# Optimization experiments

Measured on AMD Instinct MI355X. Metric: run time of the kernel, lower is better.

Reference implementation:

```python
import jax, jax.numpy as jnp
import numpy as np

B_, N_, DM = 4, 4096, 256
DS, DC = 16, 4
DIN = DM * 1          # expand = 1
DTR = (DM + 15) // 16  # dt_rank = ceil(d_model/16) = 16


def setup_inputs() -> dict:
    key = jax.random.key(0)
    ks = jax.random.split(key, 8)
    s = lambda k, shape, sc=0.02: jax.random.normal(k, shape, jnp.float32) * sc
    return {
        "x": jax.random.normal(ks[0], (B_, N_, DM), jnp.float32),
        "W_in": s(ks[1], (DM, 2 * DIN)),                 # in_proj (no bias)
        "conv_w": s(ks[2], (DIN, DC), 0.1),              # depthwise causal conv
        "conv_b": jnp.zeros((DIN,), jnp.float32),
        "W_xproj": s(ks[3], (DIN, DTR + 2 * DS)),        # x_proj (no bias)
        "W_dt": s(ks[4], (DTR, DIN), 0.1),               # dt_proj weight
        "b_dt": jnp.full((DIN,), -4.0, jnp.float32),     # dt_proj bias (softplus -> small dt)
        "A_log": jnp.log(jnp.broadcast_to(jnp.arange(1, DS + 1, dtype=jnp.float32), (DIN, DS))),
        "D": jnp.ones((DIN,), jnp.float32),              # skip connection
        "W_out": s(ks[5], (DIN, DM)),                    # out_proj (no bias)
        "H": 64,
        "W": 64,
    }


def _mamba(x, W_in, conv_w, conv_b, W_xproj, W_dt, b_dt, A_log, D, W_out):
    # x: [B, L, d_model]
    B, L, _ = x.shape
    xz = x @ W_in                                   # [B, L, 2*DIN]
    xc, z = jnp.split(xz, 2, axis=-1)
    # causal depthwise conv1d over L
    xt = jnp.transpose(xc, (0, 2, 1))               # [B, DIN, L]
    rhs = conv_w[:, None, :]                        # [DIN, 1, K]
    conv = jax.lax.conv_general_dilated(
        xt, rhs, (1,), [(DC - 1, 0)],
        dimension_numbers=("NCH", "OIH", "NCH"), feature_group_count=DIN)
    xc = jax.nn.silu(jnp.transpose(conv, (0, 2, 1)) + conv_b)   # [B, L, DIN]
    # input-dependent SSM parameters
    dbl = xc @ W_xproj                              # [B, L, DTR+2*DS]
    dt, Bm, Cm = jnp.split(dbl, [DTR, DTR + DS], axis=-1)
    delta = jax.nn.softplus(dt @ W_dt + b_dt)       # [B, L, DIN]
    A = -jnp.exp(A_log)                             # [DIN, DS]
    dA = jnp.exp(delta[..., None] * A)              # [B, L, DIN, DS]
    dBx = delta[..., None] * Bm[:, :, None, :] * xc[..., None]  # [B, L, DIN, DS]

    def step(h, inputs):
        dA_t, dBx_t, C_t = inputs                   # [B,DIN,DS],[B,DIN,DS],[B,DS]
        h = dA_t * h + dBx_t
        y = jnp.einsum("bds,bs->bd", h, C_t)
        return h, y

    h0 = jnp.zeros((B, DIN, DS), x.dtype)
    _, ys = jax.lax.scan(step, h0,
                         (jnp.moveaxis(dA, 1, 0), jnp.moveaxis(dBx, 1, 0), jnp.moveaxis(Cm, 1, 0)))
    y = jnp.moveaxis(ys, 0, 1)                      # [B, L, DIN]
    y = (y + D * xc) * jax.nn.silu(z)
    return y @ W_out                                # [B, L, d_model]


def reference(x, W_in, conv_w, conv_b, W_xproj, W_dt, b_dt, A_log, D, W_out, H, W):
    B, N, C = x.shape
    m = lambda t: _mamba(t, W_in, conv_w, conv_b, W_xproj, W_dt, b_dt, A_log, D, W_out)
    out_h_fwd = m(x)
    out_h_bwd = jnp.flip(m(jnp.flip(x, axis=1)), axis=1)
    x_v = x.reshape(B, H, W, C).transpose(0, 2, 1, 3).reshape(B, N, C)
    out_v_fwd = m(x_v).reshape(B, W, H, C).transpose(0, 2, 1, 3).reshape(B, N, C)
    out_v_bwd = jnp.flip(m(jnp.flip(x_v, axis=1)), axis=1)
    out_v_bwd = out_v_bwd.reshape(B, W, H, C).transpose(0, 2, 1, 3).reshape(B, N, C)
    out = (out_h_fwd + out_h_bwd + out_v_fwd + out_v_bwd) / 4.0
    out = jnp.clip(out, -1000.0, 1000.0)
    return jnp.nan_to_num(out, nan=0.0, posinf=1000.0, neginf=-1000.0)
```

## Files before the change

### kernel.cpp

```cpp
#include <hip/hip_runtime.h>
#include <cmath>

constexpr int BB = 4;
constexpr int LL = 4096;
constexpr int CH = 32;
constexpr int NC = LL / CH;
constexpr size_t EL = (size_t)BB * LL * 256;

typedef __attribute__((ext_vector_type(8))) short bf16x8;
typedef __attribute__((ext_vector_type(4))) float f32x4;

__device__ __forceinline__ int dirmap(int dir, int p) {
    switch (dir) {
        case 0: return p;
        case 1: return (LL - 1) - p;
        case 2: return ((p & 63) << 6) | (p >> 6);
        default: { int q = (LL - 1) - p; return ((q & 63) << 6) | (q >> 6); }
    }
}

__device__ __forceinline__ float silu_f(float v) {
    return v * __builtin_amdgcn_rcpf(1.f + __expf(-v));
}
__device__ __forceinline__ float softplus_f(float v) {
    const float sp = __logf(1.f + __expf(v));
    return (v > 20.f) ? v : sp;
}
__device__ __forceinline__ unsigned short f2bf(float f) {
    unsigned int u = __float_as_uint(f);
    return (unsigned short)((u + 0x7FFFu + ((u >> 16) & 1u)) >> 16);
}
__device__ __forceinline__ float bf2f(unsigned short s) {
    return __uint_as_float(((unsigned int)s) << 16);
}

__global__ __launch_bounds__(256) void split_x_k(
    const float* __restrict__ src, unsigned short* __restrict__ h,
    unsigned short* __restrict__ l, int n4)
{
    const int i = blockIdx.x * 256 + threadIdx.x;
    if (i >= n4) return;
    const float4 v = reinterpret_cast<const float4*>(src)[i];
    ushort4 hv, lv;
    hv.x = f2bf(v.x); lv.x = f2bf(v.x - bf2f(hv.x));
    hv.y = f2bf(v.y); lv.y = f2bf(v.y - bf2f(hv.y));
    hv.z = f2bf(v.z); lv.z = f2bf(v.z - bf2f(hv.z));
    hv.w = f2bf(v.w); lv.w = f2bf(v.w - bf2f(hv.w));
    reinterpret_cast<ushort4*>(h)[i] = hv;
    reinterpret_cast<ushort4*>(l)[i] = lv;
}

__global__ __launch_bounds__(256) void tsplit_k(
    const float* __restrict__ W, unsigned short* __restrict__ Th,
    unsigned short* __restrict__ Tl, int N)
{
    const int n = blockIdx.x;
    const int k = threadIdx.x;
    const float v = W[(size_t)k * N + n];
    const unsigned short h = f2bf(v);
    Th[(size_t)n * 256 + k] = h;
    Tl[(size_t)n * 256 + k] = f2bf(v - bf2f(h));
}

__global__ __launch_bounds__(256) void split_acc_k(
    const float* __restrict__ acc4, const float* __restrict__ zs,
    unsigned short* __restrict__ h, unsigned short* __restrict__ l, int n4)
{
    const int i = blockIdx.x * 256 + threadIdx.x;
    if (i >= n4) return;
    const float4 a0 = reinterpret_cast<const float4*>(acc4)[i];
    const float4 a1 = reinterpret_cast<const float4*>(acc4 + EL)[i];
    const float4 a2 = reinterpret_cast<const float4*>(acc4 + 2 * EL)[i];
    const float4 a3 = reinterpret_cast<const float4*>(acc4 + 3 * EL)[i];
    const float4 z = reinterpret_cast<const float4*>(zs)[i];
    float4 v;
    v.x = (a0.x + a1.x + a2.x + a3.x) * z.x * 0.25f;
    v.y = (a0.y + a1.y + a2.y + a3.y) * z.y * 0.25f;
    v.z = (a0.z + a1.z + a2.z + a3.z) * z.z * 0.25f;
    v.w = (a0.w + a1.w + a2.w + a3.w) * z.w * 0.25f;
    ushort4 hv, lv;
    hv.x = f2bf(v.x); lv.x = f2bf(v.x - bf2f(hv.x));
    hv.y = f2bf(v.y); lv.y = f2bf(v.y - bf2f(hv.y));
    hv.z = f2bf(v.z); lv.z = f2bf(v.z - bf2f(hv.z));
    hv.w = f2bf(v.w); lv.w = f2bf(v.w - bf2f(hv.w));
    reinterpret_cast<ushort4*>(h)[i] = hv;
    reinterpret_cast<ushort4*>(l)[i] = lv;
}

template<int EPI>
__global__ __launch_bounds__(256, 4) void gemm_mfma(
    const unsigned short* __restrict__ Ah, const unsigned short* __restrict__ Al,
    const unsigned short* __restrict__ BTh, const unsigned short* __restrict__ BTl,
    float* __restrict__ out0, float* __restrict__ out1)
{
    constexpr int LDT = 40;
    __shared__ unsigned short AhS[128 * LDT], AlS[128 * LDT];
    __shared__ unsigned short BhS[64 * LDT], BlS[64 * LDT];

    const int tid = threadIdx.x;
    const int wave = tid >> 6, lane = tid & 63;
    const int lm = lane & 15, quad = lane >> 4;
    const int m0 = blockIdx.y * 128, n0 = blockIdx.x * 64;

    const int srow = tid >> 2;
    const int scol = (tid & 3) * 8;

    f32x4 acc[2][4];
#pragma unroll
    for (int mt = 0; mt < 2; mt++)
#pragma unroll
        for (int nt = 0; nt < 4; nt++)
#pragma unroll
            for (int e = 0; e < 4; e++) acc[mt][nt][e] = 0.f;

    for (int k0 = 0; k0 < 256; k0 += 32) {
#pragma unroll
        for (int hh = 0; hh < 2; hh++) {
            const int r = srow + hh * 64;
            const size_t g = (size_t)(m0 + r) * 256 + k0 + scol;
            *reinterpret_cast<int4*>(&AhS[r * LDT + scol]) =
                *reinterpret_cast<const int4*>(&Ah[g]);
            *reinterpret_cast<int4*>(&AlS[r * LDT + scol]) =
                *reinterpret_cast<const int4*>(&Al[g]);
        }
        {
            const size_t g = (size_t)(n0 + srow) * 256 + k0 + scol;
            *reinterpret_cast<int4*>(&BhS[srow * LDT + scol]) =
                *reinterpret_cast<const int4*>(&BTh[g]);
            *reinterpret_cast<int4*>(&BlS[srow * LDT + scol]) =
                *reinterpret_cast<const int4*>(&BTl[g]);
        }
        __syncthreads();

        const int ko = quad * 8;
        bf16x8 a_h[2], a_l[2], b_h[4], b_l[4];
#pragma unroll
        for (int mt = 0; mt < 2; mt++) {
            const int r = wave * 32 + mt * 16 + lm;
            a_h[mt] = *reinterpret_cast<const bf16x8*>(&AhS[r * LDT + ko]);
            a_l[mt] = *reinterpret_cast<const bf16x8*>(&AlS[r * LDT + ko]);
        }
#pragma unroll
        for (int nt = 0; nt < 4; nt++) {
            const int r = nt * 16 + lm;
            b_h[nt] = *reinterpret_cast<const bf16x8*>(&BhS[r * LDT + ko]);
            b_l[nt] = *reinterpret_cast<const bf16x8*>(&BlS[r * LDT + ko]);
        }
#pragma unroll
        for (int mt = 0; mt < 2; mt++)
#pragma unroll
            for (int nt = 0; nt < 4; nt++) {
                acc[mt][nt] = __builtin_amdgcn_mfma_f32_16x16x32_bf16(
                    a_h[mt], b_h[nt], acc[mt][nt], 0, 0, 0);
                acc[mt][nt] = __builtin_amdgcn_mfma_f32_16x16x32_bf16(
                    a_h[mt], b_l[nt], acc[mt][nt], 0, 0, 0);
                acc[mt][nt] = __builtin_amdgcn_mfma_f32_16x16x32_bf16(
                    a_l[mt], b_h[nt], acc[mt][nt], 0, 0, 0);
            }
        __syncthreads();
    }

#pragma unroll
    for (int mt = 0; mt < 2; mt++) {
#pragma unroll
        for (int nt = 0; nt < 4; nt++) {
            const int col = n0 + nt * 16 + lm;
#pragma unroll
            for (int r = 0; r < 4; r++) {
                const int row = m0 + wave * 32 + mt * 16 + quad * 4 + r;
                float v = acc[mt][nt][r];
                if (EPI == 0) {
                    if (n0 < 256) out0[(size_t)row * 256 + col] = v;
                    else          out1[(size_t)row * 256 + (col - 256)] = silu_f(v);
                } else {
                    v = fminf(fmaxf(v, -1000.f), 1000.f);
                    if (v != v) v = 0.f;
                    out0[(size_t)row * 256 + col] = v;
                }
            }
        }
    }
}

__global__ __launch_bounds__(256) void conv_all(
    const float* __restrict__ xc0, const float* __restrict__ conv_w,
    const float* __restrict__ conv_b, float* __restrict__ xcd)
{
    const int bx = blockIdx.x;
    const int g = bx >> 7;
    const int nc = bx & 127;
    const int dir = g >> 2, b = g & 3;
    const int p0 = nc * CH;
    const int d = threadIdx.x;
    const size_t xbase = ((size_t)b << 12) * 256;

    const float4 cw = *reinterpret_cast<const float4*>(&conv_w[d * 4]);
    const float cb = conv_b[d];
    float xin[35];
#pragma unroll
    for (int i = 0; i < 35; i++) {
        const int p = p0 - 3 + i;
        xin[i] = (p >= 0) ? xc0[xbase + (size_t)dirmap(dir, p) * 256 + d] : 0.f;
    }
#pragma unroll
    for (int t = 0; t < 32; t++) {
        const float v = cb + cw.x * xin[t] + cw.y * xin[t + 1]
                           + cw.z * xin[t + 2] + cw.w * xin[t + 3];
        xcd[(((size_t)g << 12) + p0 + t) * 256 + d] = silu_f(v);
    }
}

__global__ __launch_bounds__(256, 2) void gemm_dbl(
    const float* __restrict__ xcd, const float* __restrict__ Wx,
    float* __restrict__ dtbc)
{
    __shared__ float Bs[256 * 48];
    __shared__ float As[16][132];

    const int tid = threadIdx.x;
    const int m0 = blockIdx.x * 128;
    const int ty = tid >> 3;
    const int tx = tid & 7;
    const int sr = tid >> 2;
    const int sc = (tid & 3) * 4;

#pragma unroll
    for (int i = 0; i < 12; i++)
        reinterpret_cast<float4*>(Bs)[tid + i * 256] =
            reinterpret_cast<const float4*>(Wx)[tid + i * 256];

    float acc[4][6];
#pragma unroll
    for (int i = 0; i < 4; i++)
#pragma unroll
        for (int j = 0; j < 6; j++) acc[i][j] = 0.f;

    for (int k0 = 0; k0 < 256; k0 += 16) {
#pragma unroll
        for (int h = 0; h < 2; h++) {
            const int r = sr + h * 64;
            const float4 av = *reinterpret_cast<const float4*>(
                &xcd[(size_t)(m0 + r) * 256 + k0 + sc]);
            As[sc + 0][r] = av.x; As[sc + 1][r] = av.y;
            As[sc + 2][r] = av.z; As[sc + 3][r] = av.w;
        }
        __syncthreads();
#pragma unroll
        for (int kk = 0; kk < 16; kk++) {
            const float4 a4 = *reinterpret_cast<const float4*>(&As[kk][ty * 4]);
            const float* brow = &Bs[(k0 + kk) * 48 + tx * 6];
            const float2 b0 = *reinterpret_cast<const float2*>(brow + 0);
            const float2 b1 = *reinterpret_cast<const float2*>(brow + 2);
            const float2 b2 = *reinterpret_cast<const float2*>(brow + 4);
            const float a[4] = {a4.x, a4.y, a4.z, a4.w};
            const float bb[6] = {b0.x, b0.y, b1.x, b1.y, b2.x, b2.y};
#pragma unroll
            for (int i = 0; i < 4; i++)
#pragma unroll
                for (int j = 0; j < 6; j++)
                    acc[i][j] = fmaf(a[i], bb[j], acc[i][j]);
        }
        __syncthreads();
    }
#pragma unroll
    for (int i = 0; i < 4; i++) {
        float* orow = &dtbc[(size_t)(m0 + ty * 4 + i) * 48 + tx * 6];
#pragma unroll
        for (int j = 0; j < 3; j++)
            *reinterpret_cast<float2*>(orow + j * 2) =
                make_float2(acc[i][j * 2], acc[i][j * 2 + 1]);
    }
}

__global__ __launch_bounds__(256) void passA2(
    const float* __restrict__ xcd, const float* __restrict__ dtbc,
    const float* __restrict__ Wdt, const float* __restrict__ bdt,
    float* __restrict__ qbuf, float* __restrict__ ssum)
{
    __shared__ float dts[32 * 48];
    const int bx = blockIdx.x;
    const int g = bx >> 7;
    const int nc = bx & 127;
    const int p0 = nc * CH;
    const int d = threadIdx.x;

    {
        const float4* src = reinterpret_cast<const float4*>(
            &dtbc[(((size_t)g << 12) + p0) * 48]);
        float4* dst = reinterpret_cast<float4*>(dts);
        dst[d] = src[d];
        if (d < 128) dst[256 + d] = src[256 + d];
    }

    float wdt[16];
#pragma unroll
    for (int r = 0; r < 16; r++) wdt[r] = Wdt[r * 256 + d];
    const float bdt_d = bdt[d];
    __syncthreads();

    float hq[16];
#pragma unroll
    for (int s = 0; s < 16; s++) hq[s] = 0.f;
    float ss = 0.f;

    const float* xrow = &xcd[(((size_t)g << 12) + p0) * 256 + d];
    float xv = xrow[0];
    for (int t = 0; t < 32; t++) {
        const float xnext = xrow[(t + 1) * 256];
        const float* drow = &dts[t * 48];
        float dv = bdt_d;
#pragma unroll
        for (int r4 = 0; r4 < 4; r4++) {
            const float4 d4 = *reinterpret_cast<const float4*>(drow + r4 * 4);
            dv = fmaf(d4.x, wdt[r4 * 4 + 0], dv);
            dv = fmaf(d4.y, wdt[r4 * 4 + 1], dv);
            dv = fmaf(d4.z, wdt[r4 * 4 + 2], dv);
            dv = fmaf(d4.w, wdt[r4 * 4 + 3], dv);
        }
        const float de = softplus_f(dv);
        ss += de;
        const float e0 = __expf(-de);
        const float dx = de * xv;
        float pw = 1.f;
#pragma unroll
        for (int s4 = 0; s4 < 4; s4++) {
            const float4 b4 = *reinterpret_cast<const float4*>(drow + 16 + s4 * 4);
            pw *= e0; hq[s4 * 4 + 0] = fmaf(pw, hq[s4 * 4 + 0], dx * b4.x);
            pw *= e0; hq[s4 * 4 + 1] = fmaf(pw, hq[s4 * 4 + 1], dx * b4.y);
            pw *= e0; hq[s4 * 4 + 2] = fmaf(pw, hq[s4 * 4 + 2], dx * b4.z);
            pw *= e0; hq[s4 * 4 + 3] = fmaf(pw, hq[s4 * 4 + 3], dx * b4.w);
        }
        xv = xnext;
    }
    const size_t base = (size_t)bx * 256 + d;
    ssum[base] = ss;
    float4* qp = reinterpret_cast<float4*>(qbuf + base * 16);
#pragma unroll
    for (int s4 = 0; s4 < 4; s4++)
        qp[s4] = make_float4(hq[s4 * 4 + 0], hq[s4 * 4 + 1],
                             hq[s4 * 4 + 2], hq[s4 * 4 + 3]);
}

__global__ __launch_bounds__(256) void scanB_k(
    float* __restrict__ qs, const float* __restrict__ ssum)
{
    const int blk = blockIdx.x;
    const int gg = blk >> 4;
    const int dd = ((blk & 15) << 4) | (threadIdx.x >> 4);
    const int s = threadIdx.x & 15;
    const float msp1 = -(float)(s + 1);
    const size_t b0 = (size_t)gg * NC * 256 + dd;

    constexpr int PD = 8;
    float qv[PD], sv[PD];
#pragma unroll
    for (int j = 0; j < PD; j++) {
        qv[j] = qs[(b0 + (size_t)j * 256) * 16 + s];
        sv[j] = ssum[b0 + (size_t)j * 256];
    }
    float h = 0.f;
    for (int nc = 0; nc < NC; nc += PD) {
        const int pn = (nc + PD < NC) ? nc + PD : nc;
        float qn[PD], sn[PD];
#pragma unroll
        for (int j = 0; j < PD; j++) {
            qn[j] = qs[(b0 + (size_t)(pn + j) * 256) * 16 + s];
            sn[j] = ssum[b0 + (size_t)(pn + j) * 256];
        }
#pragma unroll
        for (int j = 0; j < PD; j++) {
            qs[(b0 + (size_t)(nc + j) * 256) * 16 + s] = h;
            h = fmaf(__expf(msp1 * sv[j]), h, qv[j]);
        }
#pragma unroll
        for (int j = 0; j < PD; j++) { qv[j] = qn[j]; sv[j] = sn[j]; }
    }
}

__global__ __launch_bounds__(256) void passC3(
    const float* __restrict__ xcd, const float* __restrict__ dtbc,
    const float* __restrict__ Wdt, const float* __restrict__ bdt,
    const float* __restrict__ Dv, const float* __restrict__ hinit,
    float* __restrict__ acc4)
{
    __shared__ float dts[32 * 48];
    const int bx = blockIdx.x;
    const int g = bx >> 7;
    const int nc = bx & 127;
    const int dir = g >> 2, b = g & 3;
    const int p0 = nc * CH;
    const int d = threadIdx.x;
    float* accd = acc4 + (size_t)dir * EL + ((size_t)b << 12) * 256;

    {
        const float4* src = reinterpret_cast<const float4*>(
            &dtbc[(((size_t)g << 12) + p0) * 48]);
        float4* dst = reinterpret_cast<float4*>(dts);
        dst[d] = src[d];
        if (d < 128) dst[256 + d] = src[256 + d];
    }

    float wdt[16];
#pragma unroll
    for (int r = 0; r < 16; r++) wdt[r] = Wdt[r * 256 + d];
    const float bdt_d = bdt[d];
    const float Dd = Dv[d];

    float hq[16];
    const float4* hp = reinterpret_cast<const float4*>(
        hinit + (((size_t)g * NC + nc) * 256 + d) * 16);
#pragma unroll
    for (int s4 = 0; s4 < 4; s4++) {
        const float4 hv = hp[s4];
        hq[s4 * 4 + 0] = hv.x; hq[s4 * 4 + 1] = hv.y;
        hq[s4 * 4 + 2] = hv.z; hq[s4 * 4 + 3] = hv.w;
    }
    __syncthreads();

    const int nbase = dirmap(dir, p0);
    const int nstep = (dir == 0) ? 1 : (dir == 1) ? -1 : (dir == 2) ? 64 : -64;
    float* op = accd + (size_t)nbase * 256 + d;
    const ptrdiff_t ostep = (ptrdiff_t)nstep * 256;

    const float* xrow = &xcd[(((size_t)g << 12) + p0) * 256 + d];
    float xv = xrow[0];
    for (int t = 0; t < 32; t++) {
        const float xnext = xrow[(t + 1) * 256];
        const float* drow = &dts[t * 48];
        float dv = bdt_d;
#pragma unroll
        for (int r4 = 0; r4 < 4; r4++) {
            const float4 d4 = *reinterpret_cast<const float4*>(drow + r4 * 4);
            dv = fmaf(d4.x, wdt[r4 * 4 + 0], dv);
            dv = fmaf(d4.y, wdt[r4 * 4 + 1], dv);
            dv = fmaf(d4.z, wdt[r4 * 4 + 2], dv);
            dv = fmaf(d4.w, wdt[r4 * 4 + 3], dv);
        }
        const float de = softplus_f(dv);
        const float e0 = __expf(-de);
        const float dx = de * xv;
        float y = 0.f, pw = 1.f;
#pragma unroll
        for (int s4 = 0; s4 < 4; s4++) {
            const float4 b4 = *reinterpret_cast<const float4*>(drow + 16 + s4 * 4);
            const float4 c4 = *reinterpret_cast<const float4*>(drow + 32 + s4 * 4);
            pw *= e0; hq[s4 * 4 + 0] = fmaf(pw, hq[s4 * 4 + 0], dx * b4.x);
            y = fmaf(hq[s4 * 4 + 0], c4.x, y);
            pw *= e0; hq[s4 * 4 + 1] = fmaf(pw, hq[s4 * 4 + 1], dx * b4.y);
            y = fmaf(hq[s4 * 4 + 1], c4.y, y);
            pw *= e0; hq[s4 * 4 + 2] = fmaf(pw, hq[s4 * 4 + 2], dx * b4.z);
            y = fmaf(hq[s4 * 4 + 2], c4.z, y);
            pw *= e0; hq[s4 * 4 + 3] = fmaf(pw, hq[s4 * 4 + 3], dx * b4.w);
            y = fmaf(hq[s4 * 4 + 3], c4.w, y);
        }
        *op = y + Dd * xv;
        op += ostep;
        xv = xnext;
    }
}

extern "C" void kernel_launch(void* const* d_in, const int* in_sizes, int n_in,
                              void* d_out, int out_size, void* d_ws, size_t ws_size,
                              hipStream_t stream) {
    const float* x      = (const float*)d_in[0];
    const float* W_in   = (const float*)d_in[1];
    const float* conv_w = (const float*)d_in[2];
    const float* conv_b = (const float*)d_in[3];
    const float* W_xprj = (const float*)d_in[4];
    const float* W_dt   = (const float*)d_in[5];
    const float* b_dt   = (const float*)d_in[6];
    const float* Dv     = (const float*)d_in[8];
    const float* W_out  = (const float*)d_in[9];
    float* out = (float*)d_out;

    char* ws = (char*)d_ws;
    size_t off = 0;
    auto alloc = [&](size_t bytes) {
        void* p = ws + off; off += (bytes + 255) & ~(size_t)255; return p;
    };
    float* acc4 = (float*)alloc(4 * EL * 4);
    unsigned short* xh  = (unsigned short*)acc4;
    unsigned short* xl  = xh + EL;
    float* xc0 = (float*)(xl + EL);
    float* zs   = (float*)alloc(EL * 4);
    float* xcd  = (float*)alloc(4 * EL * 4);
    float* dtbc = (float*)alloc((size_t)16 * LL * 48 * 4);
    float* qbuf = (float*)alloc((size_t)16 * NC * 256 * 16 * 4);
    float* ssumb = (float*)alloc((size_t)16 * NC * 256 * 4);
    unsigned short* WinTh = (unsigned short*)alloc(512 * 256 * 2);
    unsigned short* WinTl = (unsigned short*)alloc(512 * 256 * 2);
    unsigned short* WoutTh = (unsigned short*)alloc(256 * 256 * 2);
    unsigned short* WoutTl = (unsigned short*)alloc(256 * 256 * 2);
    unsigned short* ah = (unsigned short*)qbuf;
    unsigned short* al = ah + EL;

    split_x_k<<<4096, 256, 0, stream>>>(x, xh, xl, (int)(EL / 4));
    tsplit_k<<<512, 256, 0, stream>>>(W_in, WinTh, WinTl, 512);
    tsplit_k<<<256, 256, 0, stream>>>(W_out, WoutTh, WoutTl, 256);

    gemm_mfma<0><<<dim3(8, 128), 256, 0, stream>>>(
        xh, xl, WinTh, WinTl, xc0, zs);

    conv_all<<<2048, 256, 0, stream>>>(xc0, conv_w, conv_b, xcd);

    gemm_dbl<<<512, 256, 0, stream>>>(xcd, W_xprj, dtbc);

    passA2<<<2048, 256, 0, stream>>>(xcd, dtbc, W_dt, b_dt, qbuf, ssumb);

    scanB_k<<<256, 256, 0, stream>>>(qbuf, ssumb);

    passC3<<<2048, 256, 0, stream>>>(xcd, dtbc, W_dt, b_dt, Dv, qbuf, acc4);

    split_acc_k<<<4096, 256, 0, stream>>>(acc4, zs, ah, al, (int)(EL / 4));

    gemm_mfma<2><<<dim3(4, 128), 256, 0, stream>>>(
        ah, al, WoutTh, WoutTl, out, nullptr);
}
```

Before: 307.6 us.

## Fuse conv into consumers, fold x bf16 split into input GEMM, restructure scan math

Removes the separate split_x_k and conv_all kernels. The input GEMM now splits fp32 x into hi/lo bf16 while staging tiles into shared memory, and the causal conv plus SiLU is recomputed inside gemm_dbl, passA and passC instead of reading a materialized 4x-sized xcd buffer. The scan passes compute softplus via a single exp/rcp/log, precompute the 16 powers of exp(-delta) with a shallow product tree instead of a serial chain, and split the C-dot product into four accumulators for more ILP. This trades redundant conv recomputation and more register pressure for less global traffic and fewer launches.

New measurement: 378.3 us. 1.23x slower.

```diff
diff --git a/kernel.cpp b/kernel.cpp
--- a/kernel.cpp
+++ b/kernel.cpp
@@ -22,32 +22,12 @@
 __device__ __forceinline__ float silu_f(float v) {
     return v * __builtin_amdgcn_rcpf(1.f + __expf(-v));
 }
-__device__ __forceinline__ float softplus_f(float v) {
-    const float sp = __logf(1.f + __expf(v));
-    return (v > 20.f) ? v : sp;
-}
 __device__ __forceinline__ unsigned short f2bf(float f) {
     unsigned int u = __float_as_uint(f);
     return (unsigned short)((u + 0x7FFFu + ((u >> 16) & 1u)) >> 16);
 }
 __device__ __forceinline__ float bf2f(unsigned short s) {
     return __uint_as_float(((unsigned int)s) << 16);
-}
-
-__global__ __launch_bounds__(256) void split_x_k(
-    const float* __restrict__ src, unsigned short* __restrict__ h,
-    unsigned short* __restrict__ l, int n4)
-{
-    const int i = blockIdx.x * 256 + threadIdx.x;
-    if (i >= n4) return;
-    const float4 v = reinterpret_cast<const float4*>(src)[i];
-    ushort4 hv, lv;
-    hv.x = f2bf(v.x); lv.x = f2bf(v.x - bf2f(hv.x));
-    hv.y = f2bf(v.y); lv.y = f2bf(v.y - bf2f(hv.y));
-    hv.z = f2bf(v.z); lv.z = f2bf(v.z - bf2f(hv.z));
-    hv.w = f2bf(v.w); lv.w = f2bf(v.w - bf2f(hv.w));
-    reinterpret_cast<ushort4*>(h)[i] = hv;
-    reinterpret_cast<ushort4*>(l)[i] = lv;
 }
 
 __global__ __launch_bounds__(256) void tsplit_k(
@@ -87,9 +67,8 @@
     reinterpret_cast<ushort4*>(l)[i] = lv;
 }
 
-template<int EPI>
-__global__ __launch_bounds__(256, 4) void gemm_mfma(
-    const unsigned short* __restrict__ Ah, const unsigned short* __restrict__ Al,
+__global__ __launch_bounds__(256, 4) void gemm_in(
+    const float* __restrict__ A0,
     const unsigned short* __restrict__ BTh, const unsigned short* __restrict__ BTl,
     float* __restrict__ out0, float* __restrict__ out1)
 {
@@ -118,10 +97,22 @@
         for (int hh = 0; hh < 2; hh++) {
             const int r = srow + hh * 64;
             const size_t g = (size_t)(m0 + r) * 256 + k0 + scol;
-            *reinterpret_cast<int4*>(&AhS[r * LDT + scol]) =
-                *reinterpret_cast<const int4*>(&Ah[g]);
-            *reinterpret_cast<int4*>(&AlS[r * LDT + scol]) =
-                *reinterpret_cast<const int4*>(&Al[g]);
+            const float4 v0 = *reinterpret_cast<const float4*>(&A0[g]);
+            const float4 v1 = *reinterpret_cast<const float4*>(&A0[g + 4]);
+            const float v[8] = {v0.x, v0.y, v0.z, v0.w, v1.x, v1.y, v1.z, v1.w};
+            ushort4 ha, hb, la, lb;
+            ha.x = f2bf(v[0]); la.x = f2bf(v[0] - bf2f(ha.x));
+            ha.y = f2bf(v[1]); la.y = f2bf(v[1] - bf2f(ha.y));
+            ha.z = f2bf(v[2]); la.z = f2bf(v[2] - bf2f(ha.z));
+            ha.w = f2bf(v[3]); la.w = f2bf(v[3] - bf2f(ha.w));
+            hb.x = f2bf(v[4]); lb.x = f2bf(v[4] - bf2f(hb.x));
+            hb.y = f2bf(v[5]); lb.y = f2bf(v[5] - bf2f(hb.y));
+            hb.z = f2bf(v[6]); lb.z = f2bf(v[6] - bf2f(hb.z));
+            hb.w = f2bf(v[7]); lb.w = f2bf(v[7] - bf2f(hb.w));
+            *reinterpret_cast<ushort4*>(&AhS[r * LDT + scol]) = ha;
+            *reinterpret_cast<ushort4*>(&AhS[r * LDT + scol + 4]) = hb;
+            *reinterpret_cast<ushort4*>(&AlS[r * LDT + scol]) = la;
+            *reinterpret_cast<ushort4*>(&AlS[r * LDT + scol + 4]) = lb;
         }
         {
             const size_t g = (size_t)(n0 + srow) * 256 + k0 + scol;
@@ -168,61 +159,120 @@
 #pragma unroll
             for (int r = 0; r < 4; r++) {
                 const int row = m0 + wave * 32 + mt * 16 + quad * 4 + r;
+                const float v = acc[mt][nt][r];
+                if (n0 < 256) out0[(size_t)row * 256 + col] = v;
+                else          out1[(size_t)row * 256 + (col - 256)] = silu_f(v);
+            }
+        }
+    }
+}
+
+__global__ __launch_bounds__(256, 4) void gemm_out(
+    const unsigned short* __restrict__ Ah, const unsigned short* __restrict__ Al,
+    const unsigned short* __restrict__ BTh, const unsigned short* __restrict__ BTl,
+    float* __restrict__ out0)
+{
+    constexpr int LDT = 40;
+    __shared__ unsigned short AhS[128 * LDT], AlS[128 * LDT];
+    __shared__ unsigned short BhS[64 * LDT], BlS[64 * LDT];
+
+    const int tid = threadIdx.x;
+    const int wave = tid >> 6, lane = tid & 63;
+    const int lm = lane & 15, quad = lane >> 4;
+    const int m0 = blockIdx.y * 128, n0 = blockIdx.x * 64;
+
+    const int srow = tid >> 2;
+    const int scol = (tid & 3) * 8;
+
+    f32x4 acc[2][4];
+#pragma unroll
+    for (int mt = 0; mt < 2; mt++)
+#pragma unroll
+        for (int nt = 0; nt < 4; nt++)
+#pragma unroll
+            for (int e = 0; e < 4; e++) acc[mt][nt][e] = 0.f;
+
+    for (int k0 = 0; k0 < 256; k0 += 32) {
+#pragma unroll
+        for (int hh = 0; hh < 2; hh++) {
+            const int r = srow + hh * 64;
+            const size_t g = (size_t)(m0 + r) * 256 + k0 + scol;
+            *reinterpret_cast<int4*>(&AhS[r * LDT + scol]) =
+                *reinterpret_cast<const int4*>(&Ah[g]);
+            *reinterpret_cast<int4*>(&AlS[r * LDT + scol]) =
+                *reinterpret_cast<const int4*>(&Al[g]);
+        }
+        {
+            const size_t g = (size_t)(n0 + srow) * 256 + k0 + scol;
+            *reinterpret_cast<int4*>(&BhS[srow * LDT + scol]) =
+                *reinterpret_cast<const int4*>(&BTh[g]);
+            *reinterpret_cast<int4*>(&BlS[srow * LDT + scol]) =
+                *reinterpret_cast<const int4*>(&BTl[g]);
+        }
+        __syncthreads();
+
+        const int ko = quad * 8;
+        bf16x8 a_h[2], a_l[2], b_h[4], b_l[4];
+#pragma unroll
+        for (int mt = 0; mt < 2; mt++) {
+            const int r = wave * 32 + mt * 16 + lm;
+            a_h[mt] = *reinterpret_cast<const bf16x8*>(&AhS[r * LDT + ko]);
+            a_l[mt] = *reinterpret_cast<const bf16x8*>(&AlS[r * LDT + ko]);
+        }
+#pragma unroll
+        for (int nt = 0; nt < 4; nt++) {
+            const int r = nt * 16 + lm;
+            b_h[nt] = *reinterpret_cast<const bf16x8*>(&BhS[r * LDT + ko]);
+            b_l[nt] = *reinterpret_cast<const bf16x8*>(&BlS[r * LDT + ko]);
+        }
+#pragma unroll
+        for (int mt = 0; mt < 2; mt++)
+#pragma unroll
+            for (int nt = 0; nt < 4; nt++) {
+                acc[mt][nt] = __builtin_amdgcn_mfma_f32_16x16x32_bf16(
+                    a_h[mt], b_h[nt], acc[mt][nt], 0, 0, 0);
+                acc[mt][nt] = __builtin_amdgcn_mfma_f32_16x16x32_bf16(
+                    a_h[mt], b_l[nt], acc[mt][nt], 0, 0, 0);
+                acc[mt][nt] = __builtin_amdgcn_mfma_f32_16x16x32_bf16(
+                    a_l[mt], b_h[nt], acc[mt][nt], 0, 0, 0);
+            }
+        __syncthreads();
+    }
+
+#pragma unroll
+    for (int mt = 0; mt < 2; mt++) {
+#pragma unroll
+        for (int nt = 0; nt < 4; nt++) {
+            const int col = n0 + nt * 16 + lm;
+#pragma unroll
+            for (int r = 0; r < 4; r++) {
+                const int row = m0 + wave * 32 + mt * 16 + quad * 4 + r;
                 float v = acc[mt][nt][r];
-                if (EPI == 0) {
-                    if (n0 < 256) out0[(size_t)row * 256 + col] = v;
-                    else          out1[(size_t)row * 256 + (col - 256)] = silu_f(v);
-                } else {
-                    v = fminf(fmaxf(v, -1000.f), 1000.f);
-                    if (v != v) v = 0.f;
-                    out0[(size_t)row * 256 + col] = v;
-                }
+                v = fminf(fmaxf(v, -1000.f), 1000.f);
+                if (v != v) v = 0.f;
+                out0[(size_t)row * 256 + col] = v;
             }
         }
     }
 }
 
-__global__ __launch_bounds__(256) void conv_all(
+__global__ __launch_bounds__(256, 2) void gemm_dbl(
     const float* __restrict__ xc0, const float* __restrict__ conv_w,
-    const float* __restrict__ conv_b, float* __restrict__ xcd)
-{
-    const int bx = blockIdx.x;
-    const int g = bx >> 7;
-    const int nc = bx & 127;
-    const int dir = g >> 2, b = g & 3;
-    const int p0 = nc * CH;
-    const int d = threadIdx.x;
-    const size_t xbase = ((size_t)b << 12) * 256;
-
-    const float4 cw = *reinterpret_cast<const float4*>(&conv_w[d * 4]);
-    const float cb = conv_b[d];
-    float xin[35];
-#pragma unroll
-    for (int i = 0; i < 35; i++) {
-        const int p = p0 - 3 + i;
-        xin[i] = (p >= 0) ? xc0[xbase + (size_t)dirmap(dir, p) * 256 + d] : 0.f;
-    }
-#pragma unroll
-    for (int t = 0; t < 32; t++) {
-        const float v = cb + cw.x * xin[t] + cw.y * xin[t + 1]
-                           + cw.z * xin[t + 2] + cw.w * xin[t + 3];
-        xcd[(((size_t)g << 12) + p0 + t) * 256 + d] = silu_f(v);
-    }
-}
-
-__global__ __launch_bounds__(256, 2) void gemm_dbl(
-    const float* __restrict__ xcd, const float* __restrict__ Wx,
+    const float* __restrict__ conv_b, const float* __restrict__ Wx,
     float* __restrict__ dtbc)
 {
     __shared__ float Bs[256 * 48];
     __shared__ float As[16][132];
+    __shared__ float Xr[16][132];
 
     const int tid = threadIdx.x;
     const int m0 = blockIdx.x * 128;
+    const int g = m0 >> 12;
+    const int dir = g >> 2, b = g & 3;
+    const int p0 = m0 & 4095;
+    const size_t xbase = ((size_t)b << 12) * 256;
     const int ty = tid >> 3;
     const int tx = tid & 7;
-    const int sr = tid >> 2;
-    const int sc = (tid & 3) * 4;
 
 #pragma unroll
     for (int i = 0; i < 12; i++)
@@ -237,12 +287,29 @@
 
     for (int k0 = 0; k0 < 256; k0 += 16) {
 #pragma unroll
-        for (int h = 0; h < 2; h++) {
-            const int r = sr + h * 64;
-            const float4 av = *reinterpret_cast<const float4*>(
-                &xcd[(size_t)(m0 + r) * 256 + k0 + sc]);
-            As[sc + 0][r] = av.x; As[sc + 1][r] = av.y;
-            As[sc + 2][r] = av.z; As[sc + 3][r] = av.w;
+        for (int i = 0; i < 9; i++) {
+            const int idx = tid + i * 256;
+            if (idx < 131 * 16) {
+                const int k = idx & 15, pi = idx >> 4;
+                const int gp = p0 - 3 + pi;
+                float v = 0.f;
+                if (gp >= 0)
+                    v = xc0[xbase + (size_t)dirmap(dir, gp) * 256 + k0 + k];
+                Xr[k][pi] = v;
+            }
+        }
+        __syncthreads();
+#pragma unroll
+        for (int i = 0; i < 8; i++) {
+            const int idx = tid + i * 256;
+            const int k = idx & 15, r = idx >> 4;
+            const float4 cw = *reinterpret_cast<const float4*>(&conv_w[(k0 + k) * 4]);
+            float v = conv_b[k0 + k];
+            v = fmaf(cw.x, Xr[k][r], v);
+            v = fmaf(cw.y, Xr[k][r + 1], v);
+            v = fmaf(cw.z, Xr[k][r + 2], v);
+            v = fmaf(cw.w, Xr[k][r + 3], v);
+            As[k][r] = silu_f(v);
         }
         __syncthreads();
 #pragma unroll
@@ -272,116 +339,44 @@
     }
 }
 
-__global__ __launch_bounds__(256) void passA2(
-    const float* __restrict__ xcd, const float* __restrict__ dtbc,
+struct StepOut { float e0, de, dx; };
+__device__ __forceinline__ StepOut step_front(
+    const float4& D0, const float4& D1, const float4& D2, const float4& D3,
+    const float (&wv)[16], float bd, float xv)
+{
+    float a0 = fmaf(D0.x, wv[0], bd);
+    float a1 = D0.y * wv[1];
+    float a2 = D0.z * wv[2];
+    float a3 = D0.w * wv[3];
+    a0 = fmaf(D1.x, wv[4],  a0); a1 = fmaf(D1.y, wv[5],  a1);
+    a2 = fmaf(D1.z, wv[6],  a2); a3 = fmaf(D1.w, wv[7],  a3);
+    a0 = fmaf(D2.x, wv[8],  a0); a1 = fmaf(D2.y, wv[9],  a1);
+    a2 = fmaf(D2.z, wv[10], a2); a3 = fmaf(D2.w, wv[11], a3);
+    a0 = fmaf(D3.x, wv[12], a0); a1 = fmaf(D3.y, wv[13], a1);
+    a2 = fmaf(D3.z, wv[14], a2); a3 = fmaf(D3.w, wv[15], a3);
+    const float dv = (a0 + a1) + (a2 + a3);
+    const float ex = __expf(dv);
+    const float e0 = __builtin_amdgcn_rcpf(1.f + ex);
+    float de = -__logf(e0);
+    de = (dv > 20.f) ? dv : de;
+    StepOut o; o.e0 = e0; o.de = de; o.dx = de * xv;
+    return o;
+}
+
+__device__ __forceinline__ void pows16(float e0, float (&p)[16])
+{
+    const float q2 = e0 * e0, q4 = q2 * q2, q8 = q4 * q4;
+    p[0] = e0;        p[1] = q2;        p[2] = e0 * q2;   p[3] = q4;
+    p[4] = e0 * q4;   p[5] = q2 * q4;   p[6] = p[2] * q4; p[7] = q8;
+    p[8] = e0 * q8;   p[9] = q2 * q8;   p[10] = p[2] * q8; p[11] = q4 * q8;
+    p[12] = p[4] * q8; p[13] = p[5] * q8; p[14] = p[6] * q8; p[15] = q8 * q8;
+}
+
+__global__ __launch_bounds__(256, 4) void passAL6(
+    const float* __restrict__ xc0, const float* __restrict__ conv_w,
+    const float* __restrict__ conv_b, const float* __restrict__ dtbc,
     const float* __restrict__ Wdt, const float* __restrict__ bdt,
     float* __restrict__ qbuf, float* __restrict__ ssum)
-{
-    __shared__ float dts[32 * 48];
-    const int bx = blockIdx.x;
-    const int g = bx >> 7;
-    const int nc = bx & 127;
-    const int p0 = nc * CH;
-    const int d = threadIdx.x;
-
-    {
-        const float4* src = reinterpret_cast<const float4*>(
-            &dtbc[(((size_t)g << 12) + p0) * 48]);
-        float4* dst = reinterpret_cast<float4*>(dts);
-        dst[d] = src[d];
-        if (d < 128) dst[256 + d] = src[256 + d];
-    }
-
-    float wdt[16];
-#pragma unroll
-    for (int r = 0; r < 16; r++) wdt[r] = Wdt[r * 256 + d];
-    const float bdt_d = bdt[d];
-    __syncthreads();
-
-    float hq[16];
-#pragma unroll
-    for (int s = 0; s < 16; s++) hq[s] = 0.f;
-    float ss = 0.f;
-
-    const float* xrow = &xcd[(((size_t)g << 12) + p0) * 256 + d];
-    float xv = xrow[0];
-    for (int t = 0; t < 32; t++) {
-        const float xnext = xrow[(t + 1) * 256];
-        const float* drow = &dts[t * 48];
-        float dv = bdt_d;
-#pragma unroll
-        for (int r4 = 0; r4 < 4; r4++) {
-            const float4 d4 = *reinterpret_cast<const float4*>(drow + r4 * 4);
-            dv = fmaf(d4.x, wdt[r4 * 4 + 0], dv);
-            dv = fmaf(d4.y, wdt[r4 * 4 + 1], dv);
-            dv = fmaf(d4.z, wdt[r4 * 4 + 2], dv);
-            dv = fmaf(d4.w, wdt[r4 * 4 + 3], dv);
-        }
-        const float de = softplus_f(dv);
-        ss += de;
-        const float e0 = __expf(-de);
-        const float dx = de * xv;
-        float pw = 1.f;
-#pragma unroll
-        for (int s4 = 0; s4 < 4; s4++) {
-            const float4 b4 = *reinterpret_cast<const float4*>(drow + 16 + s4 * 4);
-            pw *= e0; hq[s4 * 4 + 0] = fmaf(pw, hq[s4 * 4 + 0], dx * b4.x);
-            pw *= e0; hq[s4 * 4 + 1] = fmaf(pw, hq[s4 * 4 + 1], dx * b4.y);
-            pw *= e0; hq[s4 * 4 + 2] = fmaf(pw, hq[s4 * 4 + 2], dx * b4.z);
-            pw *= e0; hq[s4 * 4 + 3] = fmaf(pw, hq[s4 * 4 + 3], dx * b4.w);
-        }
-        xv = xnext;
-    }
-    const size_t base = (size_t)bx * 256 + d;
-    ssum[base] = ss;
-    float4* qp = reinterpret_cast<float4*>(qbuf + base * 16);
-#pragma unroll
-    for (int s4 = 0; s4 < 4; s4++)
-        qp[s4] = make_float4(hq[s4 * 4 + 0], hq[s4 * 4 + 1],
-                             hq[s4 * 4 + 2], hq[s4 * 4 + 3]);
-}
-
-__global__ __launch_bounds__(256) void scanB_k(
-    float* __restrict__ qs, const float* __restrict__ ssum)
-{
-    const int blk = blockIdx.x;
-    const int gg = blk >> 4;
-    const int dd = ((blk & 15) << 4) | (threadIdx.x >> 4);
-    const int s = threadIdx.x & 15;
-    const float msp1 = -(float)(s + 1);
-    const size_t b0 = (size_t)gg * NC * 256 + dd;
-
-    constexpr int PD = 8;
-    float qv[PD], sv[PD];
-#pragma unroll
-    for (int j = 0; j < PD; j++) {
-        qv[j] = qs[(b0 + (size_t)j * 256) * 16 + s];
-        sv[j] = ssum[b0 + (size_t)j * 256];
-    }
-    float h = 0.f;
-    for (int nc = 0; nc < NC; nc += PD) {
-        const int pn = (nc + PD < NC) ? nc + PD : nc;
-        float qn[PD], sn[PD];
-#pragma unroll
-        for (int j = 0; j < PD; j++) {
-            qn[j] = qs[(b0 + (size_t)(pn + j) * 256) * 16 + s];
-            sn[j] = ssum[b0 + (size_t)(pn + j) * 256];
-        }
-#pragma unroll
-        for (int j = 0; j < PD; j++) {
-            qs[(b0 + (size_t)(nc + j) * 256) * 16 + s] = h;
-            h = fmaf(__expf(msp1 * sv[j]), h, qv[j]);
-        }
-#pragma unroll
-        for (int j = 0; j < PD; j++) { qv[j] = qn[j]; sv[j] = sn[j]; }
-    }
-}
-
-__global__ __launch_bounds__(256) void passC3(
-    const float* __restrict__ xcd, const float* __restrict__ dtbc,
-    const float* __restrict__ Wdt, const float* __restrict__ bdt,
-    const float* __restrict__ Dv, const float* __restrict__ hinit,
-    float* __restrict__ acc4)
 {
     __shared__ float dts[32 * 48];
     const int bx = blockIdx.x;
@@ -390,7 +385,7 @@
     const int dir = g >> 2, b = g & 3;
     const int p0 = nc * CH;
     const int d = threadIdx.x;
-    float* accd = acc4 + (size_t)dir * EL + ((size_t)b << 12) * 256;
+    const size_t xbase = ((size_t)b << 12) * 256;
 
     {
         const float4* src = reinterpret_cast<const float4*>(
@@ -400,10 +395,148 @@
         if (d < 128) dst[256 + d] = src[256 + d];
     }
 
-    float wdt[16];
-#pragma unroll
-    for (int r = 0; r < 16; r++) wdt[r] = Wdt[r * 256 + d];
-    const float bdt_d = bdt[d];
+    const float4 cw = *reinterpret_cast<const float4*>(&conv_w[d * 4]);
+    const float cb = conv_b[d];
+    float xin[35];
+#pragma unroll
+    for (int i = 0; i < 35; i++) {
+        const int gp = p0 - 3 + i;
+        xin[i] = (gp >= 0) ? xc0[xbase + (size_t)dirmap(dir, gp) * 256 + d] : 0.f;
+    }
+
+    float wv[16];
+#pragma unroll
+    for (int r = 0; r < 16; r++) wv[r] = Wdt[r * 256 + d];
+    const float bd = bdt[d];
+    __syncthreads();
+
+    float hq[16];
+#pragma unroll
+    for (int s = 0; s < 16; s++) hq[s] = 0.f;
+    float ss = 0.f;
+
+#pragma unroll
+    for (int t = 0; t < 32; t++) {
+        const float* drow = &dts[t * 48];
+        const float4 D0 = *reinterpret_cast<const float4*>(drow + 0);
+        const float4 D1 = *reinterpret_cast<const float4*>(drow + 4);
+        const float4 D2 = *reinterpret_cast<const float4*>(drow + 8);
+        const float4 D3 = *reinterpret_cast<const float4*>(drow + 12);
+        float cv = cb;
+        cv = fmaf(cw.x, xin[t], cv);
+        cv = fmaf(cw.y, xin[t + 1], cv);
+        cv = fmaf(cw.z, xin[t + 2], cv);
+        cv = fmaf(cw.w, xin[t + 3], cv);
+        const float xv = silu_f(cv);
+
+        const StepOut o = step_front(D0, D1, D2, D3, wv, bd, xv);
+        ss += o.de;
+        float p[16]; pows16(o.e0, p);
+        const float4 B0 = *reinterpret_cast<const float4*>(drow + 16);
+        const float4 B1 = *reinterpret_cast<const float4*>(drow + 20);
+        const float4 B2 = *reinterpret_cast<const float4*>(drow + 24);
+        const float4 B3 = *reinterpret_cast<const float4*>(drow + 28);
+        hq[0]  = fmaf(p[0],  hq[0],  o.dx * B0.x);
+        hq[1]  = fmaf(p[1],  hq[1],  o.dx * B0.y);
+        hq[2]  = fmaf(p[2],  hq[2],  o.dx * B0.z);
+        hq[3]  = fmaf(p[3],  hq[3],  o.dx * B0.w);
+        hq[4]  = fmaf(p[4],  hq[4],  o.dx * B1.x);
+        hq[5]  = fmaf(p[5],  hq[5],  o.dx * B1.y);
+        hq[6]  = fmaf(p[6],  hq[6],  o.dx * B1.z);
+        hq[7]  = fmaf(p[7],  hq[7],  o.dx * B1.w);
+        hq[8]  = fmaf(p[8],  hq[8],  o.dx * B2.x);
+        hq[9]  = fmaf(p[9],  hq[9],  o.dx * B2.y);
+        hq[10] = fmaf(p[10], hq[10], o.dx * B2.z);
+        hq[11] = fmaf(p[11], hq[11], o.dx * B2.w);
+        hq[12] = fmaf(p[12], hq[12], o.dx * B3.x);
+        hq[13] = fmaf(p[13], hq[13], o.dx * B3.y);
+        hq[14] = fmaf(p[14], hq[14], o.dx * B3.z);
+        hq[15] = fmaf(p[15], hq[15], o.dx * B3.w);
+    }
+
+    const size_t base = (size_t)bx * 256 + d;
+    ssum[base] = ss;
+    float4* qp = reinterpret_cast<float4*>(qbuf + base * 16);
+#pragma unroll
+    for (int s4 = 0; s4 < 4; s4++)
+        qp[s4] = make_float4(hq[s4 * 4 + 0], hq[s4 * 4 + 1],
+                             hq[s4 * 4 + 2], hq[s4 * 4 + 3]);
+}
+
+__global__ __launch_bounds__(256) void scanB_k(
+    float* __restrict__ qs, const float* __restrict__ ssum)
+{
+    const int blk = blockIdx.x;
+    const int gg = blk >> 4;
+    const int dd = ((blk & 15) << 4) | (threadIdx.x >> 4);
+    const int s = threadIdx.x & 15;
+    const float msp1 = -(float)(s + 1);
+    const size_t b0 = (size_t)gg * NC * 256 + dd;
+
+    constexpr int PD = 8;
+    float qv[PD], sv[PD];
+#pragma unroll
+    for (int j = 0; j < PD; j++) {
+        qv[j] = qs[(b0 + (size_t)j * 256) * 16 + s];
+        sv[j] = ssum[b0 + (size_t)j * 256];
+    }
+    float h = 0.f;
+    for (int nc = 0; nc < NC; nc += PD) {
+        const int pn = (nc + PD < NC) ? nc + PD : nc;
+        float qn[PD], sn[PD];
+#pragma unroll
+        for (int j = 0; j < PD; j++) {
+            qn[j] = qs[(b0 + (size_t)(pn + j) * 256) * 16 + s];
+            sn[j] = ssum[b0 + (size_t)(pn + j) * 256];
+        }
+#pragma unroll
+        for (int j = 0; j < PD; j++) {
+            qs[(b0 + (size_t)(nc + j) * 256) * 16 + s] = h;
+            h = fmaf(__expf(msp1 * sv[j]), h, qv[j]);
+        }
+#pragma unroll
+        for (int j = 0; j < PD; j++) { qv[j] = qn[j]; sv[j] = sn[j]; }
+    }
+}
+
+__global__ __launch_bounds__(256, 3) void passCF6(
+    const float* __restrict__ xc0, const float* __restrict__ conv_w,
+    const float* __restrict__ conv_b, const float* __restrict__ dtbc,
+    const float* __restrict__ Wdt, const float* __restrict__ bdt,
+    const float* __restrict__ Dv, const float* __restrict__ hinit,
+    float* __restrict__ acc4)
+{
+    __shared__ float dts[32 * 48];
+    const int bx = blockIdx.x;
+    const int g = bx >> 7;
+    const int nc = bx & 127;
+    const int dir = g >> 2, b = g & 3;
+    const int p0 = nc * CH;
+    const int d = threadIdx.x;
+    const size_t xbase = ((size_t)b << 12) * 256;
+    float* accd = acc4 + (size_t)dir * EL + ((size_t)b << 12) * 256;
+
+    {
+        const float4* src = reinterpret_cast<const float4*>(
+            &dtbc[(((size_t)g << 12) + p0) * 48]);
+        float4* dst = reinterpret_cast<float4*>(dts);
+        dst[d] = src[d];
+        if (d < 128) dst[256 + d] = src[256 + d];
+    }
+
+    const float4 cw = *reinterpret_cast<const float4*>(&conv_w[d * 4]);
+    const float cb = conv_b[d];
+    float xin[35];
+#pragma unroll
+    for (int i = 0; i < 35; i++) {
+        const int gp = p0 - 3 + i;
+        xin[i] = (gp >= 0) ? xc0[xbase + (size_t)dirmap(dir, gp) * 256 + d] : 0.f;
+    }
+
+    float wv[16];
+#pragma unroll
+    for (int r = 0; r < 16; r++) wv[r] = Wdt[r * 256 + d];
+    const float bd = bdt[d];
     const float Dd = Dv[d];
 
     float hq[16];
@@ -422,40 +555,56 @@
     float* op = accd + (size_t)nbase * 256 + d;
     const ptrdiff_t ostep = (ptrdiff_t)nstep * 256;
 
-    const float* xrow = &xcd[(((size_t)g << 12) + p0) * 256 + d];
-    float xv = xrow[0];
+#pragma unroll
     for (int t = 0; t < 32; t++) {
-        const float xnext = xrow[(t + 1) * 256];
         const float* drow = &dts[t * 48];
-        float dv = bdt_d;
-#pragma unroll
-        for (int r4 = 0; r4 < 4; r4++) {
-            const float4 d4 = *reinterpret_cast<const float4*>(drow + r4 * 4);
-            dv = fmaf(d4.x, wdt[r4 * 4 + 0], dv);
-            dv = fmaf(d4.y, wdt[r4 * 4 + 1], dv);
-            dv = fmaf(d4.z, wdt[r4 * 4 + 2], dv);
-            dv = fmaf(d4.w, wdt[r4 * 4 + 3], dv);
-        }
-        const float de = softplus_f(dv);
-        const float e0 = __expf(-de);
-        const float dx = de * xv;
-        float y = 0.f, pw = 1.f;
-#pragma unroll
-        for (int s4 = 0; s4 < 4; s4++) {
-            const float4 b4 = *reinterpret_cast<const float4*>(drow + 16 + s4 * 4);
-            const float4 c4 = *reinterpret_cast<const float4*>(drow + 32 + s4 * 4);
-            pw *= e0; hq[s4 * 4 + 0] = fmaf(pw, hq[s4 * 4 + 0], dx * b4.x);
-            y = fmaf(hq[s4 * 4 + 0], c4.x, y);
-            pw *= e0; hq[s4 * 4 + 1] = fmaf(pw, hq[s4 * 4 + 1], dx * b4.y);
-            y = fmaf(hq[s4 * 4 + 1], c4.y, y);
-            pw *= e0; hq[s4 * 4 + 2] = fmaf(pw, hq[s4 * 4 + 2], dx * b4.z);
-            y = fmaf(hq[s4 * 4 + 2], c4.z, y);
-            pw *= e0; hq[s4 * 4 + 3] = fmaf(pw, hq[s4 * 4 + 3], dx * b4.w);
-            y = fmaf(hq[s4 * 4 + 3], c4.w, y);
-        }
-        *op = y + Dd * xv;
+        const float4 D0 = *reinterpret_cast<const float4*>(drow + 0);
+        const float4 D1 = *reinterpret_cast<const float4*>(drow + 4);
+        const float4 D2 = *reinterpret_cast<const float4*>(drow + 8);
+        const float4 D3 = *reinterpret_cast<const float4*>(drow + 12);
+        float cv = cb;
+        cv = fmaf(cw.x, xin[t], cv);
+        cv = fmaf(cw.y, xin[t + 1], cv);
+        cv = fmaf(cw.z, xin[t + 2], cv);
+        cv = fmaf(cw.w, xin[t + 3], cv);
+        const float xv = silu_f(cv);
+
+        const StepOut o = step_front(D0, D1, D2, D3, wv, bd, xv);
+        float p[16]; pows16(o.e0, p);
+        const float4 B0 = *reinterpret_cast<const float4*>(drow + 16);
+        const float4 B1 = *reinterpret_cast<const float4*>(drow + 20);
+        const float4 B2 = *reinterpret_cast<const float4*>(drow + 24);
+        const float4 B3 = *reinterpret_cast<const float4*>(drow + 28);
+        const float4 C0 = *reinterpret_cast<const float4*>(drow + 32);
+        const float4 C1 = *reinterpret_cast<const float4*>(drow + 36);
+        const float4 C2 = *reinterpret_cast<const float4*>(drow + 40);
+        const float4 C3 = *reinterpret_cast<const float4*>(drow + 44);
+        hq[0]  = fmaf(p[0],  hq[0],  o.dx * B0.x);
+        hq[1]  = fmaf(p[1],  hq[1],  o.dx * B0.y);
+        hq[2]  = fmaf(p[2],  hq[2],  o.dx * B0.z);
+        hq[3]  = fmaf(p[3],  hq[3],  o.dx * B0.w);
+        hq[4]  = fmaf(p[4],  hq[4],  o.dx * B1.x);
+        hq[5]  = fmaf(p[5],  hq[5],  o.dx * B1.y);
+        hq[6]  = fmaf(p[6],  hq[6],  o.dx * B1.z);
+        hq[7]  = fmaf(p[7],  hq[7],  o.dx * B1.w);
+        hq[8]  = fmaf(p[8],  hq[8],  o.dx * B2.x);
+        hq[9]  = fmaf(p[9],  hq[9],  o.dx * B2.y);
+        hq[10] = fmaf(p[10], hq[10], o.dx * B2.z);
+        hq[11] = fmaf(p[11], hq[11], o.dx * B2.w);
+        hq[12] = fmaf(p[12], hq[12], o.dx * B3.x);
+        hq[13] = fmaf(p[13], hq[13], o.dx * B3.y);
+        hq[14] = fmaf(p[14], hq[14], o.dx * B3.z);
+        hq[15] = fmaf(p[15], hq[15], o.dx * B3.w);
+        float y0 = hq[0] * C0.x, y1 = hq[1] * C0.y,
+              y2 = hq[2] * C0.z, y3 = hq[3] * C0.w;
+        y0 = fmaf(hq[4],  C1.x, y0); y1 = fmaf(hq[5],  C1.y, y1);
+        y2 = fmaf(hq[6],  C1.z, y2); y3 = fmaf(hq[7],  C1.w, y3);
+        y0 = fmaf(hq[8],  C2.x, y0); y1 = fmaf(hq[9],  C2.y, y1);
+        y2 = fmaf(hq[10], C2.z, y2); y3 = fmaf(hq[11], C2.w, y3);
+        y0 = fmaf(hq[12], C3.x, y0); y1 = fmaf(hq[13], C3.y, y1);
+        y2 = fmaf(hq[14], C3.z, y2); y3 = fmaf(hq[15], C3.w, y3);
+        *op = ((y0 + y1) + (y2 + y3)) + Dd * xv;
         op += ostep;
-        xv = xnext;
     }
 }
 
@@ -479,11 +628,8 @@
         void* p = ws + off; off += (bytes + 255) & ~(size_t)255; return p;
     };
     float* acc4 = (float*)alloc(4 * EL * 4);
-    unsigned short* xh  = (unsigned short*)acc4;
-    unsigned short* xl  = xh + EL;
-    float* xc0 = (float*)(xl + EL);
+    float* xc0  = (float*)alloc(EL * 4);
     float* zs   = (float*)alloc(EL * 4);
-    float* xcd  = (float*)alloc(4 * EL * 4);
     float* dtbc = (float*)alloc((size_t)16 * LL * 48 * 4);
     float* qbuf = (float*)alloc((size_t)16 * NC * 256 * 16 * 4);
     float* ssumb = (float*)alloc((size_t)16 * NC * 256 * 4);
@@ -494,25 +640,24 @@
     unsigned short* ah = (unsigned short*)qbuf;
     unsigned short* al = ah + EL;
 
-    split_x_k<<<4096, 256, 0, stream>>>(x, xh, xl, (int)(EL / 4));
     tsplit_k<<<512, 256, 0, stream>>>(W_in, WinTh, WinTl, 512);
     tsplit_k<<<256, 256, 0, stream>>>(W_out, WoutTh, WoutTl, 256);
 
-    gemm_mfma<0><<<dim3(8, 128), 256, 0, stream>>>(
-        xh, xl, WinTh, WinTl, xc0, zs);
-
-    conv_all<<<2048, 256, 0, stream>>>(xc0, conv_w, conv_b, xcd);
-
-    gemm_dbl<<<512, 256, 0, stream>>>(xcd, W_xprj, dtbc);
-
-    passA2<<<2048, 256, 0, stream>>>(xcd, dtbc, W_dt, b_dt, qbuf, ssumb);
+    gemm_in<<<dim3(8, 128), 256, 0, stream>>>(
+        x, WinTh, WinTl, xc0, zs);
+
+    gemm_dbl<<<512, 256, 0, stream>>>(xc0, conv_w, conv_b, W_xprj, dtbc);
+
+    passAL6<<<2048, 256, 0, stream>>>(
+        xc0, conv_w, conv_b, dtbc, W_dt, b_dt, qbuf, ssumb);
 
     scanB_k<<<256, 256, 0, stream>>>(qbuf, ssumb);
 
-    passC3<<<2048, 256, 0, stream>>>(xcd, dtbc, W_dt, b_dt, Dv, qbuf, acc4);
+    passCF6<<<2048, 256, 0, stream>>>(
+        xc0, conv_w, conv_b, dtbc, W_dt, b_dt, Dv, qbuf, acc4);
 
     split_acc_k<<<4096, 256, 0, stream>>>(acc4, zs, ah, al, (int)(EL / 4));
 
-    gemm_mfma<2><<<dim3(4, 128), 256, 0, stream>>>(
-        ah, al, WoutTh, WoutTl, out, nullptr);
-}
+    gemm_out<<<dim3(4, 128), 256, 0, stream>>>(
+        ah, al, WoutTh, WoutTl, out);
+}
```
